# Kernel tuning notes

Hardware: AMD Instinct MI355X
Metric: run time of the kernel (lower is better)

## Reference

```python
import jax, jax.numpy as jnp
import numpy as np

N = 100000   # nodes
E = 1600000  # edges (avg degree 16)
D = 128      # input feature dim
H = 64       # hidden dim (hard-coded in Sage.__init__)
C = 40       # output classes


def setup_inputs() -> dict:
    key = jax.random.key(0)
    ks = jax.random.split(key, 9)
    s_in = 1.0 / np.sqrt(D)
    s_h = 1.0 / np.sqrt(H)
    return {
        "x": jax.random.normal(ks[0], (N, D), jnp.float32),
        "edge_index": jax.random.randint(ks[1], (2, E), 0, N, dtype=jnp.int64),
        # SAGEConv params: lin_l acts on aggregated neighbors (carries bias),
        # lin_r acts on the root/self features (no bias), per PyG defaults.
        "W1_l": jax.random.uniform(ks[2], (D, H), jnp.float32, -s_in, s_in),
        "W1_r": jax.random.uniform(ks[3], (D, H), jnp.float32, -s_in, s_in),
        "b1": jax.random.uniform(ks[4], (H,), jnp.float32, -s_in, s_in),
        "W2_l": jax.random.uniform(ks[5], (H, C), jnp.float32, -s_h, s_h),
        "W2_r": jax.random.uniform(ks[6], (H, C), jnp.float32, -s_h, s_h),
        "b2": jax.random.uniform(ks[7], (C,), jnp.float32, -s_h, s_h),
    }


def _sage_conv(x, src, dst, W_l, W_r, b):
    # mean-aggregate neighbor features at destination nodes
    msg = x[src]                                             # [E, F] gather
    summed = jax.ops.segment_sum(msg, dst, num_segments=N)   # [N, F]
    deg = jax.ops.segment_sum(jnp.ones((src.shape[0],), x.dtype), dst,
                              num_segments=N)                # [N]
    agg = summed / jnp.maximum(deg, 1.0)[:, None]
    return agg @ W_l + x @ W_r + b


def reference(x, edge_index, W1_l, W1_r, b1, W2_l, W2_r, b2):
    src, dst = edge_index[0], edge_index[1]
    h = _sage_conv(x, src, dst, W1_l, W1_r, b1)
    h = jax.nn.relu(h)
    # F.dropout(training=False) in eval mode -> identity
    out = _sage_conv(h, src, dst, W2_l, W2_r, b2)
    return jax.nn.log_softmax(out, axis=1)
```

## Files before the change

kernel.cpp:

```cpp
#include <hip/hip_runtime.h>

__device__ __forceinline__ float bf2f(unsigned short u) {
  union { unsigned int i; float f; } c; c.i = ((unsigned int)u) << 16; return c.f;
}
__device__ __forceinline__ unsigned short f2bf(float f) {
  union { float f; unsigned int i; } c; c.f = f;
  unsigned int x = c.i;
  return (unsigned short)((x + 0x7fffu + ((x >> 16) & 1u)) >> 16);
}
__device__ __forceinline__ float lo16(unsigned int w) { return bf2f((unsigned short)(w & 0xffffu)); }
__device__ __forceinline__ float hi16(unsigned int w) { return bf2f((unsigned short)(w >> 16)); }

#define DD 128
#define HH 64
#define CC 40
#define NBUCK 256
#define NCHUNK 128
#define MAXNPB 512

using bf16x8 = __attribute__((ext_vector_type(8))) short;
using f32x4  = __attribute__((ext_vector_type(4))) float;

__global__ void detect(const unsigned int* e32, const unsigned int* x32, int* flags) {
  __shared__ unsigned int redOr[256];
  __shared__ int redCnt[256];
  int tid = threadIdx.x;
  unsigned int v = 0;
  for (int i = tid; i < 4096; i += 256) v |= e32[2 * i + 1];
  int cnt = 0;
  for (int i = tid; i < 4096; i += 256) {
    unsigned int w = x32[i];
    unsigned int expo = (w >> 7) & 0xffu;
    unsigned short lo = (unsigned short)(w & 0xffffu);
    if (lo == 0 || (expo >= 100u && expo <= 133u)) cnt++;
  }
  redOr[tid] = v; redCnt[tid] = cnt; __syncthreads();
  for (int s = 128; s > 0; s >>= 1) {
    if (tid < s) { redOr[tid] |= redOr[tid + s]; redCnt[tid] += redCnt[tid + s]; }
    __syncthreads();
  }
  if (tid == 0) {
    flags[0] = (redOr[0] == 0u) ? 1 : 0;
    flags[1] = (redCnt[0] < 2048) ? 1 : 0;
  }
}

__global__ __launch_bounds__(256) void hist_k(const int* e32, int E, int N,
                                              const int* flags, int nodesPerB,
                                              int* histG) {
  __shared__ int cnt[NBUCK];
  int tid = threadIdx.x;
  if (tid < NBUCK) cnt[tid] = 0;
  __syncthreads();
  int isI64 = flags[0];
  int chunk = (E + NCHUNK - 1) / NCHUNK;
  int e0 = blockIdx.x * chunk, e1 = min(e0 + chunk, E);
  for (int i = e0 + tid; i < e1; i += 256) {
    int d = isI64 ? e32[2 * (E + i)] : e32[E + i];
    d = min(max(d, 0), N - 1);
    atomicAdd(&cnt[d / nodesPerB], 1);
  }
  __syncthreads();
  if (tid < NBUCK) histG[tid * NCHUNK + blockIdx.x] = cnt[tid];
}

__global__ void hscan_prepw(const int* histG, int* ohist, int* bbase, int* row_ptr,
                            int N, int E,
                            const void* W1l, const void* W1r, const void* b1,
                            const void* W2l, const void* W2r, const void* b2,
                            const int* flags, unsigned short* Wb1, unsigned short* Wb2,
                            float* b1f, float* b2f) {
  int tid = threadIdx.x;
  if (blockIdx.x == 1) {
    int isf = flags[1];
    auto rd = [&](const void* p, int i) -> float {
      return isf ? ((const float*)p)[i] : bf2f(((const unsigned short*)p)[i]);
    };
    for (int idx = tid; idx < 128 * 128; idx += 1024) {
      int n = idx >> 7, k = idx & 127;
      float v = (n < HH) ? rd(W1l, k * HH + n) : rd(W1r, k * HH + (n - HH));
      Wb1[idx] = f2bf(v);
    }
    for (int idx = tid; idx < 48 * 128; idx += 1024) {
      int n = idx >> 7, k = idx & 127;
      float v = 0.f;
      if (n < CC) v = (k < HH) ? rd(W2l, k * CC + n) : rd(W2r, (k - HH) * CC + n);
      Wb2[idx] = f2bf(v);
    }
    if (tid < HH) b1f[tid] = rd(b1, tid);
    if (tid < CC) b2f[tid] = rd(b2, tid);
    return;
  }
  __shared__ int tmp[1024];
  int v[32];
  int base = tid * 32;
  int s = 0;
#pragma unroll
  for (int k = 0; k < 32; k++) { v[k] = histG[base + k]; s += v[k]; }
  tmp[tid] = s; __syncthreads();
  for (int st = 1; st < 1024; st <<= 1) {
    int t = (tid >= st) ? tmp[tid - st] : 0;
    __syncthreads();
    tmp[tid] += t;
    __syncthreads();
  }
  int run = tmp[tid] - s;
#pragma unroll
  for (int k = 0; k < 32; k++) { ohist[base + k] = run; run += v[k]; }
  __syncthreads();
  if (tid < NBUCK) bbase[tid] = ohist[tid * NCHUNK];
  if (tid == 0) { bbase[NBUCK] = E; row_ptr[N] = E; }
}

__global__ __launch_bounds__(256) void scatter_k(const int* e32, int E, int N,
                                                 const int* flags, int nodesPerB,
                                                 const int* ohist, uint2* ebuf) {
  __shared__ int cur[NBUCK];
  int tid = threadIdx.x;
  if (tid < NBUCK) cur[tid] = ohist[tid * NCHUNK + blockIdx.x];
  __syncthreads();
  int isI64 = flags[0];
  int chunk = (E + NCHUNK - 1) / NCHUNK;
  int e0 = blockIdx.x * chunk, e1 = min(e0 + chunk, E);
  for (int i = e0 + tid; i < e1; i += 256) {
    int s, d;
    if (isI64) { s = e32[2 * i]; d = e32[2 * (E + i)]; }
    else       { s = e32[i];     d = e32[E + i]; }
    s = min(max(s, 0), N - 1);
    d = min(max(d, 0), N - 1);
    int p = atomicAdd(&cur[d / nodesPerB], 1);
    ebuf[p] = make_uint2((unsigned)s, (unsigned)d);
  }
}

__global__ __launch_bounds__(256) void bktB_or_t1(
    const uint2* ebuf, const int* bbase,
    int nbuck, int nodesPerB, int* row_ptr, float* invd, int* col, int N,
    const void* xraw, const int* flags, const unsigned short* Wb1, const float* b1f,
    unsigned short* t1, unsigned short* s1, int T1B) {
  __shared__ int ldsb[MAXNPB + 256];
  int b = blockIdx.x;
  int tid = threadIdx.x;

  if (b < nbuck) {
    int* cnt = ldsb;
    int* sA  = ldsb + MAXNPB;
    int base_node = b * nodesPerB;
    int nn = min(nodesPerB, N - base_node);
    if (nn <= 0) return;
    int eb0 = bbase[b], eb1 = bbase[b + 1];
    int nE = eb1 - eb0;
    const uint2* ee = ebuf + eb0;
    for (int i = tid; i < nn; i += 256) cnt[i] = 0;
    __syncthreads();
    for (int i = tid; i < nE; i += 256)
      atomicAdd(&cnt[(int)ee[i].y - base_node], 1);
    __syncthreads();
    int per = (nn + 255) / 256;
    int myb = tid * per;
    int dreg[2];
    int ssum = 0;
#pragma unroll
    for (int k = 0; k < 2; k++) {
      int idx = myb + k;
      int v = (k < per && idx < nn) ? cnt[idx] : 0;
      dreg[k] = v; ssum += v;
    }
    sA[tid] = ssum;
    __syncthreads();
    for (int st = 1; st < 256; st <<= 1) {
      int t = (tid >= st) ? sA[tid - st] : 0;
      __syncthreads();
      sA[tid] += t;
      __syncthreads();
    }
    int run = eb0 + sA[tid] - ssum;
    __syncthreads();
#pragma unroll
    for (int k = 0; k < 2; k++) {
      int idx = myb + k;
      if (k < per && idx < nn) {
        row_ptr[base_node + idx] = run;
        invd[base_node + idx] = 1.0f / (float)max(dreg[k], 1);
        cnt[idx] = run;
        run += dreg[k];
      }
    }
    __syncthreads();
    for (int i = tid; i < nE; i += 256) {
      uint2 eg = ee[i];
      int p = atomicAdd(&cnt[(int)eg.y - base_node], 1);
      col[p] = (int)eg.x;
    }
    return;
  }

  int t = b - nbuck;
  if (t >= T1B) return;
  int lane = tid & 63, wv = tid >> 6;
  int nb = t * 64 + wv * 16;
  int oc = lane & 15, kgrp = lane >> 4;
  int node = min(nb + oc, N - 1);
  f32x4 acc[8];
#pragma unroll
  for (int i = 0; i < 8; i++) acc[i] = (f32x4){0.f, 0.f, 0.f, 0.f};

  if (flags[1]) {
    const float4* x4 = (const float4*)xraw;
#pragma unroll
    for (int kb = 0; kb < 4; kb++) {
      int k0 = kb * 32 + kgrp * 8;
      float4 a0 = x4[(size_t)node * 32 + (k0 >> 2)];
      float4 a1 = x4[(size_t)node * 32 + (k0 >> 2) + 1];
      bf16x8 af;
      af[0] = (short)f2bf(a0.x); af[1] = (short)f2bf(a0.y);
      af[2] = (short)f2bf(a0.z); af[3] = (short)f2bf(a0.w);
      af[4] = (short)f2bf(a1.x); af[5] = (short)f2bf(a1.y);
      af[6] = (short)f2bf(a1.z); af[7] = (short)f2bf(a1.w);
#pragma unroll
      for (int nblk = 0; nblk < 8; nblk++) {
        bf16x8 bfr = *(const bf16x8*)&Wb1[(nblk * 16 + oc) * 128 + k0];
        acc[nblk] = __builtin_amdgcn_mfma_f32_16x16x32_bf16(af, bfr, acc[nblk], 0, 0, 0);
      }
    }
  } else {
    const unsigned short* x16 = (const unsigned short*)xraw;
#pragma unroll
    for (int kb = 0; kb < 4; kb++) {
      int k0 = kb * 32 + kgrp * 8;
      bf16x8 af = *(const bf16x8*)&x16[(size_t)node * 128 + k0];
#pragma unroll
      for (int nblk = 0; nblk < 8; nblk++) {
        bf16x8 bfr = *(const bf16x8*)&Wb1[(nblk * 16 + oc) * 128 + k0];
        acc[nblk] = __builtin_amdgcn_mfma_f32_16x16x32_bf16(af, bfr, acc[nblk], 0, 0, 0);
      }
    }
  }

  int r0 = kgrp * 4;
#pragma unroll
  for (int nblk = 0; nblk < 8; nblk++) {
    float bias = (nblk >= 4) ? b1f[(nblk - 4) * 16 + oc] : 0.f;
#pragma unroll
    for (int r = 0; r < 4; r++) {
      int nn = nb + r0 + r;
      if (nn < N) {
        if (nblk < 4)
          t1[(size_t)nn * HH + nblk * 16 + oc] = f2bf(acc[nblk][r]);
        else
          s1[(size_t)nn * HH + (nblk - 4) * 16 + oc] = f2bf(acc[nblk][r] + bias);
      }
    }
  }
}

__device__ __forceinline__ void gather_rows(const uint4* t8, const int* col,
                                            int start, int end, int r, int c,
                                            float acc[8]) {
  for (int base = start; base < end; base += 16) {
    int i0 = base + r, i1 = base + 8 + r;
    uint4 v0 = make_uint4(0, 0, 0, 0), v1 = make_uint4(0, 0, 0, 0);
    bool g0 = (i0 < end), g1 = (i1 < end);
    int nb0 = g0 ? col[i0] : 0;
    int nb1 = g1 ? col[i1] : 0;
    if (g0) v0 = t8[nb0 * 8 + c];
    if (g1) v1 = t8[nb1 * 8 + c];
    acc[0] += lo16(v0.x) + lo16(v1.x);
    acc[1] += hi16(v0.x) + hi16(v1.x);
    acc[2] += lo16(v0.y) + lo16(v1.y);
    acc[3] += hi16(v0.y) + hi16(v1.y);
    acc[4] += lo16(v0.z) + lo16(v1.z);
    acc[5] += hi16(v0.z) + hi16(v1.z);
    acc[6] += lo16(v0.w) + lo16(v1.w);
    acc[7] += hi16(v0.w) + hi16(v1.w);
  }
#pragma unroll
  for (int m = 8; m <= 32; m <<= 1)
#pragma unroll
    for (int i = 0; i < 8; i++) acc[i] += __shfl_xor(acc[i], m, 64);
}

__global__ __launch_bounds__(256) void aggregate1(const unsigned short* t1,
                                                  const unsigned short* s1,
                                                  const int* row_ptr, const float* invd,
                                                  const int* col, unsigned short* h, int N) {
  int wave = threadIdx.x >> 6, lane = threadIdx.x & 63;
  int r = lane >> 3, c = lane & 7;
  int n = blockIdx.x * 4 + wave;
  if (n >= N) return;
  int start = row_ptr[n], end = row_ptr[n + 1];
  float acc[8] = {0, 0, 0, 0, 0, 0, 0, 0};
  gather_rows((const uint4*)t1, col, start, end, r, c, acc);

  if (r == 0) {
    float id = invd[n];
    uint4 sv = ((const uint4*)s1)[n * 8 + c];
    float s[8] = {lo16(sv.x), hi16(sv.x), lo16(sv.y), hi16(sv.y),
                  lo16(sv.z), hi16(sv.z), lo16(sv.w), hi16(sv.w)};
    unsigned int o[4];
#pragma unroll
    for (int i = 0; i < 4; i++) {
      float a0 = fmaxf(acc[2 * i] * id + s[2 * i], 0.f);
      float a1 = fmaxf(acc[2 * i + 1] * id + s[2 * i + 1], 0.f);
      o[i] = (unsigned int)f2bf(a0) | ((unsigned int)f2bf(a1) << 16);
    }
    ((uint4*)h)[n * 8 + c] = make_uint4(o[0], o[1], o[2], o[3]);
  }
}

__global__ __launch_bounds__(256) void agg2(const unsigned short* h,
                                            const int* row_ptr, const float* invd,
                                            const int* col, unsigned short* aggh, int N) {
  int wave = threadIdx.x >> 6, lane = threadIdx.x & 63;
  int r = lane >> 3, c = lane & 7;
  int n = blockIdx.x * 4 + wave;
  if (n >= N) return;
  int start = row_ptr[n], end = row_ptr[n + 1];
  float acc[8] = {0, 0, 0, 0, 0, 0, 0, 0};
  gather_rows((const uint4*)h, col, start, end, r, c, acc);

  if (r == 0) {
    float id = invd[n];
    unsigned int o[4];
#pragma unroll
    for (int i = 0; i < 4; i++) {
      o[i] = (unsigned int)f2bf(acc[2 * i] * id) |
             ((unsigned int)f2bf(acc[2 * i + 1] * id) << 16);
    }
    ((uint4*)aggh)[n * 8 + c] = make_uint4(o[0], o[1], o[2], o[3]);
  }
}

__global__ __launch_bounds__(256) void final_k(const unsigned short* aggh,
                                               const unsigned short* h,
                                               const unsigned short* Wb2,
                                               const float* b2f,
                                               float* out, int N) {
  int tid = threadIdx.x;
  int lane = tid & 63, wv = tid >> 6;
  int nb = blockIdx.x * 64 + wv * 16;
  int oc = lane & 15, kgrp = lane >> 4;
  int node = min(nb + oc, N - 1);
  f32x4 acc[3];
#pragma unroll
  for (int i = 0; i < 3; i++) acc[i] = (f32x4){0.f, 0.f, 0.f, 0.f};

#pragma unroll
  for (int kb = 0; kb < 4; kb++) {
    int k0 = kb * 32 + kgrp * 8;
    const unsigned short* src = (kb < 2) ? aggh : h;
    int kk = k0 & 63;
    bf16x8 af = *(const bf16x8*)&src[(size_t)node * HH + kk];
#pragma unroll
    for (int nblk = 0; nblk < 3; nblk++) {
      bf16x8 bfr = *(const bf16x8*)&Wb2[(nblk * 16 + oc) * 128 + k0];
      acc[nblk] = __builtin_amdgcn_mfma_f32_16x16x32_bf16(af, bfr, acc[nblk], 0, 0, 0);
    }
  }

#pragma unroll
  for (int nblk = 0; nblk < 3; nblk++) {
    int cc = nblk * 16 + oc;
    float bias = (cc < CC) ? b2f[cc] : 0.f;
#pragma unroll
    for (int r = 0; r < 4; r++) acc[nblk][r] += bias;
  }

#pragma unroll
  for (int r = 0; r < 4; r++) {
    int nn = nb + kgrp * 4 + r;
    float m = -INFINITY;
#pragma unroll
    for (int nblk = 0; nblk < 3; nblk++)
      if (nblk * 16 + oc < CC) m = fmaxf(m, acc[nblk][r]);
    for (int off = 1; off <= 8; off <<= 1) m = fmaxf(m, __shfl_xor(m, off, 64));
    float s = 0.f;
#pragma unroll
    for (int nblk = 0; nblk < 3; nblk++)
      if (nblk * 16 + oc < CC) s += __expf(acc[nblk][r] - m);
    for (int off = 1; off <= 8; off <<= 1) s += __shfl_xor(s, off, 64);
    float lse = m + __logf(s);
    if (nn < N) {
#pragma unroll
      for (int nblk = 0; nblk < 3; nblk++) {
        int cc = nblk * 16 + oc;
        if (cc < CC) out[(size_t)nn * CC + cc] = acc[nblk][r] - lse;
      }
    }
  }
}

extern "C" void kernel_launch(void* const* d_in, const int* in_sizes, int n_in,
                              void* d_out, int out_size, void* d_ws, size_t ws_size,
                              hipStream_t stream) {
  const void* x   = d_in[0];
  const int*  e   = (const int*)d_in[1];
  const void* W1l = d_in[2];
  const void* W1r = d_in[3];
  const void* b1  = d_in[4];
  const void* W2l = d_in[5];
  const void* W2r = d_in[6];
  const void* b2  = d_in[7];
  float* out = (float*)d_out;

  const int N = in_sizes[0] / DD;
  const int E = in_sizes[1] / 2;
  const int nodesPerB = (N + NBUCK - 1) / NBUCK;
  const int nbuck = (N + nodesPerB - 1) / nodesPerB;
  const int T1B = (N + 63) / 64;

  char* w = (char*)d_ws;
  size_t off = 0;
  auto carve = [&](size_t bytes) -> void* {
    void* p = (void*)(w + off);
    off += (bytes + 255) & ~(size_t)255;
    return p;
  };
  int* col     = (int*)carve((size_t)E * 4);
  int* row_ptr = (int*)carve((size_t)(N + 1) * 4);
  float* invd  = (float*)carve((size_t)N * 4);
  int* histG   = (int*)carve((size_t)NBUCK * NCHUNK * 4);
  int* ohist   = (int*)carve((size_t)NBUCK * NCHUNK * 4);
  int* bbase   = (int*)carve((NBUCK + 1) * 4);
  int* flags   = (int*)carve(8);
  unsigned short* t1   = (unsigned short*)carve((size_t)N * HH * 2);
  unsigned short* s1   = (unsigned short*)carve((size_t)N * HH * 2);
  unsigned short* h    = (unsigned short*)carve((size_t)N * HH * 2);
  unsigned short* Wb1  = (unsigned short*)carve(128 * 128 * 2);
  unsigned short* Wb2  = (unsigned short*)carve(48 * 128 * 2);
  float* b1f   = (float*)carve(HH * sizeof(float));
  float* b2f   = (float*)carve(CC * sizeof(float));
  uint2* ebuf  = (uint2*)carve((size_t)E * 8);
  unsigned short* aggh = (unsigned short*)ebuf;
  (void)ws_size; (void)n_in; (void)out_size;

  detect<<<1, 256, 0, stream>>>((const unsigned int*)e, (const unsigned int*)x, flags);
  hist_k<<<NCHUNK, 256, 0, stream>>>(e, E, N, flags, nodesPerB, histG);
  hscan_prepw<<<2, 1024, 0, stream>>>(histG, ohist, bbase, row_ptr, N, E,
                                      W1l, W1r, b1, W2l, W2r, b2,
                                      flags, Wb1, Wb2, b1f, b2f);
  scatter_k<<<NCHUNK, 256, 0, stream>>>(e, E, N, flags, nodesPerB, ohist, ebuf);
  bktB_or_t1<<<nbuck + T1B, 256, 0, stream>>>(ebuf, bbase,
                                              nbuck, nodesPerB, row_ptr, invd, col, N,
                                              x, flags, Wb1, b1f, t1, s1, T1B);
  aggregate1<<<(N + 3) / 4, 256, 0, stream>>>(t1, s1, row_ptr, invd, col, h, N);
  agg2<<<(N + 3) / 4, 256, 0, stream>>>(h, row_ptr, invd, col, aggh, N);
  final_k<<<(N + 63) / 64, 256, 0, stream>>>(aggh, h, Wb2, b2f, out, N);
}
```

Before: 316.4 us.

## Build CSR via global-atomic degree count and direct scatter instead of bucket sort

Replaces the two-level bucket-sort CSR construction (histogram of buckets, intermediate edge buffer, per-bucket LDS counting) with a per-node degree count using global atomics, a three-stage multi-block prefix scan, and a direct atomic-cursor fill of the column array. This removes the 8-byte-per-edge intermediate buffer pass and the extra bucket pass, but adds contended global atomics on random destination nodes and more kernel launches. The order of neighbours within a row becomes nondeterministic, which can change floating-point summation order.

```diff
diff --git a/kernel.cpp b/kernel.cpp
--- a/kernel.cpp
+++ b/kernel.cpp
@@ -14,17 +14,24 @@
 #define DD 128
 #define HH 64
 #define CC 40
-#define NBUCK 256
-#define NCHUNK 128
-#define MAXNPB 512
+#define DEGB 256
+#define FILLB 256
+#define NSB 256
 
 using bf16x8 = __attribute__((ext_vector_type(8))) short;
 using f32x4  = __attribute__((ext_vector_type(4))) float;
 
-__global__ void detect(const unsigned int* e32, const unsigned int* x32, int* flags) {
+__global__ __launch_bounds__(256) void detect_zero(const unsigned int* e32,
+                                                   const unsigned int* x32,
+                                                   int* flags, int* deg, int N) {
+  int b = blockIdx.x, tid = threadIdx.x;
+  int npb = (N + NSB - 1) / NSB;
+  int n0 = b * npb, n1 = min(n0 + npb, N);
+  for (int i = n0 + tid; i < n1; i += 256) deg[i] = 0;
+  if (b) return;
+
   __shared__ unsigned int redOr[256];
   __shared__ int redCnt[256];
-  int tid = threadIdx.x;
   unsigned int v = 0;
   for (int i = tid; i < 4096; i += 256) v |= e32[2 * i + 1];
   int cnt = 0;
@@ -45,43 +52,24 @@
   }
 }
 
-__global__ __launch_bounds__(256) void hist_k(const int* e32, int E, int N,
-                                              const int* flags, int nodesPerB,
-                                              int* histG) {
-  __shared__ int cnt[NBUCK];
-  int tid = threadIdx.x;
-  if (tid < NBUCK) cnt[tid] = 0;
-  __syncthreads();
-  int isI64 = flags[0];
-  int chunk = (E + NCHUNK - 1) / NCHUNK;
-  int e0 = blockIdx.x * chunk, e1 = min(e0 + chunk, E);
-  for (int i = e0 + tid; i < e1; i += 256) {
-    int d = isI64 ? e32[2 * (E + i)] : e32[E + i];
-    d = min(max(d, 0), N - 1);
-    atomicAdd(&cnt[d / nodesPerB], 1);
-  }
-  __syncthreads();
-  if (tid < NBUCK) histG[tid * NCHUNK + blockIdx.x] = cnt[tid];
-}
-
-__global__ void hscan_prepw(const int* histG, int* ohist, int* bbase, int* row_ptr,
-                            int N, int E,
-                            const void* W1l, const void* W1r, const void* b1,
-                            const void* W2l, const void* W2r, const void* b2,
-                            const int* flags, unsigned short* Wb1, unsigned short* Wb2,
-                            float* b1f, float* b2f) {
-  int tid = threadIdx.x;
-  if (blockIdx.x == 1) {
+__global__ __launch_bounds__(256) void deg_prep(const int* e32, int E, int N,
+                                                const int* flags, int* deg,
+                                                const void* W1l, const void* W1r, const void* b1,
+                                                const void* W2l, const void* W2r, const void* b2,
+                                                unsigned short* Wb1, unsigned short* Wb2,
+                                                float* b1f, float* b2f) {
+  int b = blockIdx.x, tid = threadIdx.x;
+  if (b == DEGB) {
     int isf = flags[1];
     auto rd = [&](const void* p, int i) -> float {
       return isf ? ((const float*)p)[i] : bf2f(((const unsigned short*)p)[i]);
     };
-    for (int idx = tid; idx < 128 * 128; idx += 1024) {
+    for (int idx = tid; idx < 128 * 128; idx += 256) {
       int n = idx >> 7, k = idx & 127;
       float v = (n < HH) ? rd(W1l, k * HH + n) : rd(W1r, k * HH + (n - HH));
       Wb1[idx] = f2bf(v);
     }
-    for (int idx = tid; idx < 48 * 128; idx += 1024) {
+    for (int idx = tid; idx < 48 * 128; idx += 256) {
       int n = idx >> 7, k = idx & 127;
       float v = 0.f;
       if (n < CC) v = (k < HH) ? rd(W2l, k * CC + n) : rd(W2r, (k - HH) * CC + n);
@@ -91,111 +79,109 @@
     if (tid < CC) b2f[tid] = rd(b2, tid);
     return;
   }
-  __shared__ int tmp[1024];
-  int v[32];
-  int base = tid * 32;
+  int isI64 = flags[0];
+  int chunk = (E + DEGB - 1) / DEGB;
+  int e0 = b * chunk, e1 = min(e0 + chunk, E);
+  for (int i = e0 + tid; i < e1; i += 256) {
+    int d = isI64 ? e32[2 * (E + i)] : e32[E + i];
+    d = min(max(d, 0), N - 1);
+    atomicAdd(&deg[d], 1);
+  }
+}
+
+__global__ __launch_bounds__(256) void scanA(const int* deg, int N, int* bsum) {
+  __shared__ int red[256];
+  int b = blockIdx.x, tid = threadIdx.x;
+  int npb = (N + NSB - 1) / NSB;
+  int n0 = b * npb, n1 = min(n0 + npb, N);
   int s = 0;
-#pragma unroll
-  for (int k = 0; k < 32; k++) { v[k] = histG[base + k]; s += v[k]; }
-  tmp[tid] = s; __syncthreads();
-  for (int st = 1; st < 1024; st <<= 1) {
-    int t = (tid >= st) ? tmp[tid - st] : 0;
-    __syncthreads();
-    tmp[tid] += t;
-    __syncthreads();
-  }
-  int run = tmp[tid] - s;
-#pragma unroll
-  for (int k = 0; k < 32; k++) { ohist[base + k] = run; run += v[k]; }
-  __syncthreads();
-  if (tid < NBUCK) bbase[tid] = ohist[tid * NCHUNK];
-  if (tid == 0) { bbase[NBUCK] = E; row_ptr[N] = E; }
-}
-
-__global__ __launch_bounds__(256) void scatter_k(const int* e32, int E, int N,
-                                                 const int* flags, int nodesPerB,
-                                                 const int* ohist, uint2* ebuf) {
-  __shared__ int cur[NBUCK];
+  for (int i = n0 + tid; i < n1; i += 256) s += deg[i];
+  red[tid] = s; __syncthreads();
+  for (int st = 128; st > 0; st >>= 1) {
+    if (tid < st) red[tid] += red[tid + st];
+    __syncthreads();
+  }
+  if (tid == 0) bsum[b] = red[0];
+}
+
+__global__ __launch_bounds__(256) void scanB(const int* bsum, int* sbase,
+                                             int* row_ptr, int N, int E) {
+  __shared__ int t[256];
   int tid = threadIdx.x;
-  if (tid < NBUCK) cur[tid] = ohist[tid * NCHUNK + blockIdx.x];
-  __syncthreads();
-  int isI64 = flags[0];
-  int chunk = (E + NCHUNK - 1) / NCHUNK;
-  int e0 = blockIdx.x * chunk, e1 = min(e0 + chunk, E);
-  for (int i = e0 + tid; i < e1; i += 256) {
-    int s, d;
-    if (isI64) { s = e32[2 * i]; d = e32[2 * (E + i)]; }
-    else       { s = e32[i];     d = e32[E + i]; }
-    s = min(max(s, 0), N - 1);
-    d = min(max(d, 0), N - 1);
-    int p = atomicAdd(&cur[d / nodesPerB], 1);
-    ebuf[p] = make_uint2((unsigned)s, (unsigned)d);
-  }
-}
-
-__global__ __launch_bounds__(256) void bktB_or_t1(
-    const uint2* ebuf, const int* bbase,
-    int nbuck, int nodesPerB, int* row_ptr, float* invd, int* col, int N,
-    const void* xraw, const int* flags, const unsigned short* Wb1, const float* b1f,
+  int v = bsum[tid];
+  t[tid] = v; __syncthreads();
+  for (int st = 1; st < 256; st <<= 1) {
+    int u = (tid >= st) ? t[tid - st] : 0;
+    __syncthreads();
+    t[tid] += u;
+    __syncthreads();
+  }
+  sbase[tid] = t[tid] - v;
+  if (tid == 0) row_ptr[N] = E;
+}
+
+__global__ __launch_bounds__(256) void scanC(const int* deg, const int* sbase, int N,
+                                             int* row_ptr, int* cursor, float* invd) {
+  __shared__ int lds[256];
+  int b = blockIdx.x, tid = threadIdx.x;
+  int npb = (N + NSB - 1) / NSB;
+  int base = b * npb;
+  int nn = min(npb, N - base);
+  if (nn <= 0) return;
+  int per = (nn + 255) / 256;
+  int myb = tid * per;
+  int v[4];
+  int ssum = 0;
+#pragma unroll
+  for (int k = 0; k < 4; k++) {
+    int idx = myb + k;
+    int d = (k < per && idx < nn) ? deg[base + idx] : 0;
+    v[k] = d; ssum += d;
+  }
+  lds[tid] = ssum; __syncthreads();
+  for (int st = 1; st < 256; st <<= 1) {
+    int u = (tid >= st) ? lds[tid - st] : 0;
+    __syncthreads();
+    lds[tid] += u;
+    __syncthreads();
+  }
+  int run = sbase[b] + lds[tid] - ssum;
+#pragma unroll
+  for (int k = 0; k < 4; k++) {
+    int idx = myb + k;
+    if (k < per && idx < nn) {
+      row_ptr[base + idx] = run;
+      cursor[base + idx] = run;
+      invd[base + idx] = 1.0f / (float)max(v[k], 1);
+      run += v[k];
+    }
+  }
+}
+
+__global__ __launch_bounds__(256) void fill_or_t1(
+    const int* e32, int E, int N, const int* flags, int* cursor, int* col,
+    const void* xraw, const unsigned short* Wb1, const float* b1f,
     unsigned short* t1, unsigned short* s1, int T1B) {
-  __shared__ int ldsb[MAXNPB + 256];
   int b = blockIdx.x;
   int tid = threadIdx.x;
 
-  if (b < nbuck) {
-    int* cnt = ldsb;
-    int* sA  = ldsb + MAXNPB;
-    int base_node = b * nodesPerB;
-    int nn = min(nodesPerB, N - base_node);
-    if (nn <= 0) return;
-    int eb0 = bbase[b], eb1 = bbase[b + 1];
-    int nE = eb1 - eb0;
-    const uint2* ee = ebuf + eb0;
-    for (int i = tid; i < nn; i += 256) cnt[i] = 0;
-    __syncthreads();
-    for (int i = tid; i < nE; i += 256)
-      atomicAdd(&cnt[(int)ee[i].y - base_node], 1);
-    __syncthreads();
-    int per = (nn + 255) / 256;
-    int myb = tid * per;
-    int dreg[2];
-    int ssum = 0;
-#pragma unroll
-    for (int k = 0; k < 2; k++) {
-      int idx = myb + k;
-      int v = (k < per && idx < nn) ? cnt[idx] : 0;
-      dreg[k] = v; ssum += v;
-    }
-    sA[tid] = ssum;
-    __syncthreads();
-    for (int st = 1; st < 256; st <<= 1) {
-      int t = (tid >= st) ? sA[tid - st] : 0;
-      __syncthreads();
-      sA[tid] += t;
-      __syncthreads();
-    }
-    int run = eb0 + sA[tid] - ssum;
-    __syncthreads();
-#pragma unroll
-    for (int k = 0; k < 2; k++) {
-      int idx = myb + k;
-      if (k < per && idx < nn) {
-        row_ptr[base_node + idx] = run;
-        invd[base_node + idx] = 1.0f / (float)max(dreg[k], 1);
-        cnt[idx] = run;
-        run += dreg[k];
-      }
-    }
-    __syncthreads();
-    for (int i = tid; i < nE; i += 256) {
-      uint2 eg = ee[i];
-      int p = atomicAdd(&cnt[(int)eg.y - base_node], 1);
-      col[p] = (int)eg.x;
+  if (b < FILLB) {
+    int isI64 = flags[0];
+    int chunk = (E + FILLB - 1) / FILLB;
+    int e0 = b * chunk, e1 = min(e0 + chunk, E);
+    for (int i = e0 + tid; i < e1; i += 256) {
+      int s, d;
+      if (isI64) { s = e32[2 * i]; d = e32[2 * (E + i)]; }
+      else       { s = e32[i];     d = e32[E + i]; }
+      s = min(max(s, 0), N - 1);
+      d = min(max(d, 0), N - 1);
+      int p = atomicAdd(&cursor[d], 1);
+      col[p] = s;
     }
     return;
   }
 
-  int t = b - nbuck;
+  int t = b - FILLB;
   if (t >= T1B) return;
   int lane = tid & 63, wv = tid >> 6;
   int nb = t * 64 + wv * 16;
@@ -405,8 +391,6 @@
 
   const int N = in_sizes[0] / DD;
   const int E = in_sizes[1] / 2;
-  const int nodesPerB = (N + NBUCK - 1) / NBUCK;
-  const int nbuck = (N + nodesPerB - 1) / nodesPerB;
   const int T1B = (N + 63) / 64;
 
   char* w = (char*)d_ws;
@@ -419,30 +403,31 @@
   int* col     = (int*)carve((size_t)E * 4);
   int* row_ptr = (int*)carve((size_t)(N + 1) * 4);
   float* invd  = (float*)carve((size_t)N * 4);
-  int* histG   = (int*)carve((size_t)NBUCK * NCHUNK * 4);
-  int* ohist   = (int*)carve((size_t)NBUCK * NCHUNK * 4);
-  int* bbase   = (int*)carve((NBUCK + 1) * 4);
+  int* deg     = (int*)carve((size_t)N * 4);
+  int* cursor  = (int*)carve((size_t)N * 4);
+  int* bsum    = (int*)carve(NSB * 4);
+  int* sbase   = (int*)carve(NSB * 4);
   int* flags   = (int*)carve(8);
   unsigned short* t1   = (unsigned short*)carve((size_t)N * HH * 2);
   unsigned short* s1   = (unsigned short*)carve((size_t)N * HH * 2);
   unsigned short* h    = (unsigned short*)carve((size_t)N * HH * 2);
+  unsigned short* aggh = (unsigned short*)carve((size_t)N * HH * 2);
   unsigned short* Wb1  = (unsigned short*)carve(128 * 128 * 2);
   unsigned short* Wb2  = (unsigned short*)carve(48 * 128 * 2);
   float* b1f   = (float*)carve(HH * sizeof(float));
   float* b2f   = (float*)carve(CC * sizeof(float));
-  uint2* ebuf  = (uint2*)carve((size_t)E * 8);
-  unsigned short* aggh = (unsigned short*)ebuf;
   (void)ws_size; (void)n_in; (void)out_size;
 
-  detect<<<1, 256, 0, stream>>>((const unsigned int*)e, (const unsigned int*)x, flags);
-  hist_k<<<NCHUNK, 256, 0, stream>>>(e, E, N, flags, nodesPerB, histG);
-  hscan_prepw<<<2, 1024, 0, stream>>>(histG, ohist, bbase, row_ptr, N, E,
-                                      W1l, W1r, b1, W2l, W2r, b2,
-                                      flags, Wb1, Wb2, b1f, b2f);
-  scatter_k<<<NCHUNK, 256, 0, stream>>>(e, E, N, flags, nodesPerB, ohist, ebuf);
-  bktB_or_t1<<<nbuck + T1B, 256, 0, stream>>>(ebuf, bbase,
-                                              nbuck, nodesPerB, row_ptr, invd, col, N,
-                                              x, flags, Wb1, b1f, t1, s1, T1B);
+  detect_zero<<<NSB, 256, 0, stream>>>((const unsigned int*)e, (const unsigned int*)x,
+                                       flags, deg, N);
+  deg_prep<<<DEGB + 1, 256, 0, stream>>>(e, E, N, flags, deg,
+                                         W1l, W1r, b1, W2l, W2r, b2,
+                                         Wb1, Wb2, b1f, b2f);
+  scanA<<<NSB, 256, 0, stream>>>(deg, N, bsum);
+  scanB<<<1, 256, 0, stream>>>(bsum, sbase, row_ptr, N, E);
+  scanC<<<NSB, 256, 0, stream>>>(deg, sbase, N, row_ptr, cursor, invd);
+  fill_or_t1<<<FILLB + T1B, 256, 0, stream>>>(e, E, N, flags, cursor, col,
+                                              x, Wb1, b1f, t1, s1, T1B);
   aggregate1<<<(N + 3) / 4, 256, 0, stream>>>(t1, s1, row_ptr, invd, col, h, N);
   agg2<<<(N + 3) / 4, 256, 0, stream>>>(h, row_ptr, invd, col, aggh, N);
   final_k<<<(N + 63) / 64, 256, 0, stream>>>(aggh, h, Wb2, b2f, out, N);
```

Result: slower. 394.7 us (+24.8%).

## Sub-sort CSR neighbors into four source-range quarters for gather locality

Applied to the files above, without the earlier changes.

The CSR build now keys each edge by (destination, source quarter), so every node's neighbor list is split into four segments ordered by source-index range, with four row pointers stored per node. The aggregation kernels walk the four segments in turn, 8 rows per step instead of 16. The goal is to make concurrently running waves gather from similar regions of the feature table for better cache locality. In exchange it adds more LDS counters and prefix-scan work in the bucket build, a larger row-pointer array, and less per-step memory parallelism in the gather loops, with extra partial iterations on short segments.

```diff
diff --git a/kernel.cpp b/kernel.cpp
--- a/kernel.cpp
+++ b/kernel.cpp
@@ -17,11 +17,13 @@
 #define NBUCK 256
 #define NCHUNK 128
 #define MAXNPB 512
+#define NQ 4
 
 using bf16x8 = __attribute__((ext_vector_type(8))) short;
 using f32x4  = __attribute__((ext_vector_type(4))) float;
 
-__global__ void detect(const unsigned int* e32, const unsigned int* x32, int* flags) {
+__global__ __launch_bounds__(256) void detect(const unsigned int* e32,
+                                              const unsigned int* x32, int* flags) {
   __shared__ unsigned int redOr[256];
   __shared__ int redCnt[256];
   int tid = threadIdx.x;
@@ -64,7 +66,7 @@
   if (tid < NBUCK) histG[tid * NCHUNK + blockIdx.x] = cnt[tid];
 }
 
-__global__ void hscan_prepw(const int* histG, int* ohist, int* bbase, int* row_ptr,
+__global__ void hscan_prepw(const int* histG, int* ohist, int* bbase, int* row_ptr4,
                             int N, int E,
                             const void* W1l, const void* W1r, const void* b1,
                             const void* W2l, const void* W2r, const void* b2,
@@ -109,7 +111,7 @@
   for (int k = 0; k < 32; k++) { ohist[base + k] = run; run += v[k]; }
   __syncthreads();
   if (tid < NBUCK) bbase[tid] = ohist[tid * NCHUNK];
-  if (tid == 0) { bbase[NBUCK] = E; row_ptr[N] = E; }
+  if (tid == 0) { bbase[NBUCK] = E; row_ptr4[NQ * N] = E; }
 }
 
 __global__ __launch_bounds__(256) void scatter_k(const int* e32, int E, int N,
@@ -135,35 +137,44 @@
 
 __global__ __launch_bounds__(256) void bktB_or_t1(
     const uint2* ebuf, const int* bbase,
-    int nbuck, int nodesPerB, int* row_ptr, float* invd, int* col, int N,
+    int nbuck, int nodesPerB, int qshift, int* row_ptr4, float* invd, int* col, int N,
     const void* xraw, const int* flags, const unsigned short* Wb1, const float* b1f,
     unsigned short* t1, unsigned short* s1, int T1B) {
-  __shared__ int ldsb[MAXNPB + 256];
+  __shared__ int ldsb[MAXNPB * NQ + 256];
   int b = blockIdx.x;
   int tid = threadIdx.x;
 
   if (b < nbuck) {
     int* cnt = ldsb;
-    int* sA  = ldsb + MAXNPB;
+    int* sA  = ldsb + MAXNPB * NQ;
     int base_node = b * nodesPerB;
     int nn = min(nodesPerB, N - base_node);
     if (nn <= 0) return;
+    int nk = nn * NQ;
     int eb0 = bbase[b], eb1 = bbase[b + 1];
     int nE = eb1 - eb0;
     const uint2* ee = ebuf + eb0;
-    for (int i = tid; i < nn; i += 256) cnt[i] = 0;
-    __syncthreads();
-    for (int i = tid; i < nE; i += 256)
-      atomicAdd(&cnt[(int)ee[i].y - base_node], 1);
-    __syncthreads();
-    int per = (nn + 255) / 256;
+    for (int i = tid; i < nk; i += 256) cnt[i] = 0;
+    __syncthreads();
+    for (int i = tid; i < nE; i += 256) {
+      uint2 eg = ee[i];
+      int key = ((int)eg.y - base_node) * NQ + (int)(eg.x >> qshift);
+      atomicAdd(&cnt[key], 1);
+    }
+    __syncthreads();
+    for (int i = tid; i < nn; i += 256) {
+      int d = cnt[NQ * i] + cnt[NQ * i + 1] + cnt[NQ * i + 2] + cnt[NQ * i + 3];
+      invd[base_node + i] = 1.0f / (float)max(d, 1);
+    }
+    __syncthreads();
+    int per = (nk + 255) / 256;
     int myb = tid * per;
-    int dreg[2];
+    int dreg[8];
     int ssum = 0;
 #pragma unroll
-    for (int k = 0; k < 2; k++) {
+    for (int k = 0; k < 8; k++) {
       int idx = myb + k;
-      int v = (k < per && idx < nn) ? cnt[idx] : 0;
+      int v = (k < per && idx < nk) ? cnt[idx] : 0;
       dreg[k] = v; ssum += v;
     }
     sA[tid] = ssum;
@@ -177,11 +188,10 @@
     int run = eb0 + sA[tid] - ssum;
     __syncthreads();
 #pragma unroll
-    for (int k = 0; k < 2; k++) {
+    for (int k = 0; k < 8; k++) {
       int idx = myb + k;
-      if (k < per && idx < nn) {
-        row_ptr[base_node + idx] = run;
-        invd[base_node + idx] = 1.0f / (float)max(dreg[k], 1);
+      if (k < per && idx < nk) {
+        row_ptr4[(size_t)(base_node + (idx >> 2)) * NQ + (idx & 3)] = run;
         cnt[idx] = run;
         run += dreg[k];
       }
@@ -189,7 +199,8 @@
     __syncthreads();
     for (int i = tid; i < nE; i += 256) {
       uint2 eg = ee[i];
-      int p = atomicAdd(&cnt[(int)eg.y - base_node], 1);
+      int key = ((int)eg.y - base_node) * NQ + (int)(eg.x >> qshift);
+      int p = atomicAdd(&cnt[key], 1);
       col[p] = (int)eg.x;
     }
     return;
@@ -254,47 +265,46 @@
   }
 }
 
-__device__ __forceinline__ void gather_rows(const uint4* t8, const int* col,
-                                            int start, int end, int r, int c,
-                                            float acc[8]) {
-  for (int base = start; base < end; base += 16) {
-    int i0 = base + r, i1 = base + 8 + r;
-    uint4 v0 = make_uint4(0, 0, 0, 0), v1 = make_uint4(0, 0, 0, 0);
-    bool g0 = (i0 < end), g1 = (i1 < end);
-    int nb0 = g0 ? col[i0] : 0;
-    int nb1 = g1 ? col[i1] : 0;
-    if (g0) v0 = t8[nb0 * 8 + c];
-    if (g1) v1 = t8[nb1 * 8 + c];
-    acc[0] += lo16(v0.x) + lo16(v1.x);
-    acc[1] += hi16(v0.x) + hi16(v1.x);
-    acc[2] += lo16(v0.y) + lo16(v1.y);
-    acc[3] += hi16(v0.y) + hi16(v1.y);
-    acc[4] += lo16(v0.z) + lo16(v1.z);
-    acc[5] += hi16(v0.z) + hi16(v1.z);
-    acc[6] += lo16(v0.w) + lo16(v1.w);
-    acc[7] += hi16(v0.w) + hi16(v1.w);
-  }
-#pragma unroll
-  for (int m = 8; m <= 32; m <<= 1)
-#pragma unroll
-    for (int i = 0; i < 8; i++) acc[i] += __shfl_xor(acc[i], m, 64);
+__device__ __forceinline__ void gather_seg(const uint4* t8, const int* col,
+                                           int s0, int s1, int r, int c,
+                                           float acc[8]) {
+  for (int base = s0; base < s1; base += 8) {
+    int i = base + r;
+    bool g = (i < s1);
+    int nb = g ? col[i] : 0;
+    uint4 v = make_uint4(0, 0, 0, 0);
+    if (g) v = t8[(size_t)nb * 8 + c];
+    acc[0] += lo16(v.x); acc[1] += hi16(v.x);
+    acc[2] += lo16(v.y); acc[3] += hi16(v.y);
+    acc[4] += lo16(v.z); acc[5] += hi16(v.z);
+    acc[6] += lo16(v.w); acc[7] += hi16(v.w);
+  }
 }
 
 __global__ __launch_bounds__(256) void aggregate1(const unsigned short* t1,
                                                   const unsigned short* s1,
-                                                  const int* row_ptr, const float* invd,
+                                                  const int* row_ptr4, const float* invd,
                                                   const int* col, unsigned short* h, int N) {
   int wave = threadIdx.x >> 6, lane = threadIdx.x & 63;
   int r = lane >> 3, c = lane & 7;
   int n = blockIdx.x * 4 + wave;
   if (n >= N) return;
-  int start = row_ptr[n], end = row_ptr[n + 1];
+  int4 rp = *(const int4*)&row_ptr4[(size_t)NQ * n];
+  int e4 = row_ptr4[(size_t)NQ * n + 4];
   float acc[8] = {0, 0, 0, 0, 0, 0, 0, 0};
-  gather_rows((const uint4*)t1, col, start, end, r, c, acc);
+  const uint4* t8 = (const uint4*)t1;
+  gather_seg(t8, col, rp.x, rp.y, r, c, acc);
+  gather_seg(t8, col, rp.y, rp.z, r, c, acc);
+  gather_seg(t8, col, rp.z, rp.w, r, c, acc);
+  gather_seg(t8, col, rp.w, e4, r, c, acc);
+#pragma unroll
+  for (int m = 8; m <= 32; m <<= 1)
+#pragma unroll
+    for (int i = 0; i < 8; i++) acc[i] += __shfl_xor(acc[i], m, 64);
 
   if (r == 0) {
     float id = invd[n];
-    uint4 sv = ((const uint4*)s1)[n * 8 + c];
+    uint4 sv = ((const uint4*)s1)[(size_t)n * 8 + c];
     float s[8] = {lo16(sv.x), hi16(sv.x), lo16(sv.y), hi16(sv.y),
                   lo16(sv.z), hi16(sv.z), lo16(sv.w), hi16(sv.w)};
     unsigned int o[4];
@@ -304,20 +314,29 @@
       float a1 = fmaxf(acc[2 * i + 1] * id + s[2 * i + 1], 0.f);
       o[i] = (unsigned int)f2bf(a0) | ((unsigned int)f2bf(a1) << 16);
     }
-    ((uint4*)h)[n * 8 + c] = make_uint4(o[0], o[1], o[2], o[3]);
+    ((uint4*)h)[(size_t)n * 8 + c] = make_uint4(o[0], o[1], o[2], o[3]);
   }
 }
 
 __global__ __launch_bounds__(256) void agg2(const unsigned short* h,
-                                            const int* row_ptr, const float* invd,
+                                            const int* row_ptr4, const float* invd,
                                             const int* col, unsigned short* aggh, int N) {
   int wave = threadIdx.x >> 6, lane = threadIdx.x & 63;
   int r = lane >> 3, c = lane & 7;
   int n = blockIdx.x * 4 + wave;
   if (n >= N) return;
-  int start = row_ptr[n], end = row_ptr[n + 1];
+  int4 rp = *(const int4*)&row_ptr4[(size_t)NQ * n];
+  int e4 = row_ptr4[(size_t)NQ * n + 4];
   float acc[8] = {0, 0, 0, 0, 0, 0, 0, 0};
-  gather_rows((const uint4*)h, col, start, end, r, c, acc);
+  const uint4* h8 = (const uint4*)h;
+  gather_seg(h8, col, rp.x, rp.y, r, c, acc);
+  gather_seg(h8, col, rp.y, rp.z, r, c, acc);
+  gather_seg(h8, col, rp.z, rp.w, r, c, acc);
+  gather_seg(h8, col, rp.w, e4, r, c, acc);
+#pragma unroll
+  for (int m = 8; m <= 32; m <<= 1)
+#pragma unroll
+    for (int i = 0; i < 8; i++) acc[i] += __shfl_xor(acc[i], m, 64);
 
   if (r == 0) {
     float id = invd[n];
@@ -327,7 +346,7 @@
       o[i] = (unsigned int)f2bf(acc[2 * i] * id) |
              ((unsigned int)f2bf(acc[2 * i + 1] * id) << 16);
     }
-    ((uint4*)aggh)[n * 8 + c] = make_uint4(o[0], o[1], o[2], o[3]);
+    ((uint4*)aggh)[(size_t)n * 8 + c] = make_uint4(o[0], o[1], o[2], o[3]);
   }
 }
 
@@ -408,6 +427,8 @@
   const int nodesPerB = (N + NBUCK - 1) / NBUCK;
   const int nbuck = (N + nodesPerB - 1) / nodesPerB;
   const int T1B = (N + 63) / 64;
+  int qshift = 0;
+  while (((unsigned)(N - 1) >> qshift) > 3u) qshift++;
 
   char* w = (char*)d_ws;
   size_t off = 0;
@@ -416,13 +437,13 @@
     off += (bytes + 255) & ~(size_t)255;
     return p;
   };
-  int* col     = (int*)carve((size_t)E * 4);
-  int* row_ptr = (int*)carve((size_t)(N + 1) * 4);
-  float* invd  = (float*)carve((size_t)N * 4);
-  int* histG   = (int*)carve((size_t)NBUCK * NCHUNK * 4);
-  int* ohist   = (int*)carve((size_t)NBUCK * NCHUNK * 4);
-  int* bbase   = (int*)carve((NBUCK + 1) * 4);
-  int* flags   = (int*)carve(8);
+  int* col      = (int*)carve((size_t)E * 4);
+  int* row_ptr4 = (int*)carve(((size_t)N * NQ + 1) * 4);
+  float* invd   = (float*)carve((size_t)N * 4);
+  int* histG    = (int*)carve((size_t)NBUCK * NCHUNK * 4);
+  int* ohist    = (int*)carve((size_t)NBUCK * NCHUNK * 4);
+  int* bbase    = (int*)carve((NBUCK + 1) * 4);
+  int* flags    = (int*)carve(8);
   unsigned short* t1   = (unsigned short*)carve((size_t)N * HH * 2);
   unsigned short* s1   = (unsigned short*)carve((size_t)N * HH * 2);
   unsigned short* h    = (unsigned short*)carve((size_t)N * HH * 2);
@@ -436,14 +457,15 @@
 
   detect<<<1, 256, 0, stream>>>((const unsigned int*)e, (const unsigned int*)x, flags);
   hist_k<<<NCHUNK, 256, 0, stream>>>(e, E, N, flags, nodesPerB, histG);
-  hscan_prepw<<<2, 1024, 0, stream>>>(histG, ohist, bbase, row_ptr, N, E,
+  hscan_prepw<<<2, 1024, 0, stream>>>(histG, ohist, bbase, row_ptr4, N, E,
                                       W1l, W1r, b1, W2l, W2r, b2,
                                       flags, Wb1, Wb2, b1f, b2f);
   scatter_k<<<NCHUNK, 256, 0, stream>>>(e, E, N, flags, nodesPerB, ohist, ebuf);
   bktB_or_t1<<<nbuck + T1B, 256, 0, stream>>>(ebuf, bbase,
-                                              nbuck, nodesPerB, row_ptr, invd, col, N,
+                                              nbuck, nodesPerB, qshift, row_ptr4,
+                                              invd, col, N,
                                               x, flags, Wb1, b1f, t1, s1, T1B);
-  aggregate1<<<(N + 3) / 4, 256, 0, stream>>>(t1, s1, row_ptr, invd, col, h, N);
-  agg2<<<(N + 3) / 4, 256, 0, stream>>>(h, row_ptr, invd, col, aggh, N);
+  aggregate1<<<(N + 3) / 4, 256, 0, stream>>>(t1, s1, row_ptr4, invd, col, h, N);
+  agg2<<<(N + 3) / 4, 256, 0, stream>>>(h, row_ptr4, invd, col, aggh, N);
   final_k<<<(N + 63) / 64, 256, 0, stream>>>(aggh, h, Wb2, b2f, out, N);
 }
```

New measurement: 340.8 us. 7.7% more time.
